# Optimization experiments

Measured on AMD Instinct MI355X. Metric: run time of the kernel, lower is better.

The kernel has to match this reference:

```python
import jax, jax.numpy as jnp
import numpy as np

SEQ, B, H, NP, HN = 2048, 2, 2048, 16, 128
SCALE = 1.0 / 11.313708498984761  # 1/sqrt(128), hardcoded in the source baddbmm


def setup_inputs() -> dict:
    key = jax.random.key(0)
    k1, k2, k3 = jax.random.split(key, 3)
    return {
        "hidden_states": jax.random.normal(k1, (SEQ, B, H), dtype=jnp.float32),
        "w_qkv": jax.random.normal(k2, (3 * H, H), dtype=jnp.float32) * 0.02,
        "w_out": jax.random.normal(k3, (H, H), dtype=jnp.float32) * 0.02,
    }


def reference(hidden_states, w_qkv, w_out):
    s, b, h = hidden_states.shape
    # QKV projection (column-parallel linear, no bias): [s, b, 3h]
    qkv = hidden_states @ w_qkv.T
    # [s, b, np, 3*hn] then split (num_query_groups == num_heads)
    qkv = qkv.reshape(s, b, NP, 3 * HN)
    q, k, v = qkv[..., :HN], qkv[..., HN:2 * HN], qkv[..., 2 * HN:]
    # baddbmm QK^T with alpha = 1/sqrt(128): scores [b, np, sq, sk]
    scores = jnp.einsum("sbnh,tbnh->bnst", q, k) * SCALE
    # scale_t == 1 then plain softmax (fallback path; no mask applied)
    prob = jax.nn.softmax(scores, axis=-1)
    # context: bmm(prob, V) -> [sq, b, np, hn] -> [sq, b, h]
    ctx = jnp.einsum("bnst,tbnh->sbnh", prob, v).reshape(s, b, h)
    # row-parallel output linear (no bias)
    return ctx @ w_out.T
```

## Files before the change

### kernel.cpp

```cpp
#include <hip/hip_runtime.h>
#include <stdint.h>

#define SEQ 2048
#define BATCH 2
#define HID 2048
#define NHEADS 16
#define HDIM 128
#define QKV_LD 6144
#define SCALE_F 0.08838834764831845f
#define LOG2E_F 1.4426950408889634f

typedef unsigned short u16;
using bf16x8 = __attribute__((ext_vector_type(8))) short;
using f32x4  = __attribute__((ext_vector_type(4))) float;

__device__ inline u16 f2bf(float f) {
  union { float f; uint32_t u; } c; c.f = f;
  uint32_t u = c.u;
  uint32_t r = (u + 0x7fffu + ((u >> 16) & 1u)) >> 16;
  return (u16)r;
}

__device__ inline void gl_lds16(const u16* g, u16* l) {
  __builtin_amdgcn_global_load_lds((const __attribute__((address_space(1))) void*)g,
                                   (__attribute__((address_space(3))) void*)l,
                                   16, 0, 0);
}

__global__ void cvt_all(const float* __restrict__ hs, const float* __restrict__ wqkv,
                        const float* __restrict__ wout, u16* __restrict__ ws_out) {
  int i = blockIdx.x * blockDim.x + threadIdx.x;
  const float* src;
  int j;
  float sc = 1.0f;
  if (i < 2097152) { src = hs; j = i; }
  else if (i < 5242880) {
    j = i - 2097152; src = wqkv;
    const int f = j >> 9;
    if ((f % 384) < 128) sc = SCALE_F;
  } else { j = i - 5242880; src = wout; }
  float4 v = ((const float4*)src)[j];
  ushort4 o;
  o.x = f2bf(v.x * sc); o.y = f2bf(v.y * sc); o.z = f2bf(v.z * sc); o.w = f2bf(v.w * sc);
  ((ushort4*)ws_out)[i] = o;
}

template<int MODE>
__global__ __launch_bounds__(256)
void gemm_bt(const u16* __restrict__ A, const u16* __restrict__ Bw,
             void* __restrict__ Cout, u16* __restrict__ vt, int M, int N, int K) {
  __shared__ __align__(16) u16 As[128 * 64];
  __shared__ __align__(16) u16 Bs[128 * 64];
  const int bm = blockIdx.x, bn = blockIdx.y;
  const int tid = threadIdx.x;
  const int wave = tid >> 6, lane = tid & 63;
  const int quad = lane >> 4, l16 = lane & 15;
  const int wm = (wave >> 1) * 64, wn = (wave & 1) * 64;
  f32x4 acc[4][4] = {};

  const u16* Ablk = A + (size_t)(bm * 128) * K;
  const u16* Bblk = Bw + (size_t)(bn * 128) * K;

  for (int k0 = 0; k0 < K; k0 += 64) {
    __syncthreads();
    #pragma unroll
    for (int p = 0; p < 4; ++p) {
      int j = p * 256 + tid;
      int r = j >> 3, cs = j & 7, c = cs ^ (r & 7);
      gl_lds16(Ablk + (size_t)r * K + k0 + c * 8, As + (p * 256 + wave * 64) * 8);
      gl_lds16(Bblk + (size_t)r * K + k0 + c * 8, Bs + (p * 256 + wave * 64) * 8);
    }
    __syncthreads();
    #pragma unroll
    for (int ks = 0; ks < 2; ++ks) {
      bf16x8 af[4], bfr[4];
      #pragma unroll
      for (int mt = 0; mt < 4; ++mt) {
        int row = wm + mt * 16 + l16;
        int cc = (ks * 4 + quad) ^ (row & 7);
        af[mt] = *(const bf16x8*)&As[(row * 8 + cc) * 8];
      }
      #pragma unroll
      for (int nt = 0; nt < 4; ++nt) {
        int row = wn + nt * 16 + l16;
        int cc = (ks * 4 + quad) ^ (row & 7);
        bfr[nt] = *(const bf16x8*)&Bs[(row * 8 + cc) * 8];
      }
      #pragma unroll
      for (int mt = 0; mt < 4; ++mt)
        #pragma unroll
        for (int nt = 0; nt < 4; ++nt)
          acc[mt][nt] = __builtin_amdgcn_mfma_f32_16x16x32_bf16(af[mt], bfr[nt], acc[mt][nt], 0, 0, 0);
    }
  }

  if (MODE == 1 && (bn % 3) == 2) {
    const int h = bn / 3;
    u16* vt0 = vt + ((size_t)h * HDIM) * SEQ;
    u16* vt1 = vt + ((size_t)(NHEADS + h) * HDIM) * SEQ;
    #pragma unroll
    for (int mt = 0; mt < 4; ++mt)
      #pragma unroll
      for (int nt = 0; nt < 4; ++nt) {
        const int hd = wn + nt * 16 + l16;
        const int s0 = (bm * 128 + wm + mt * 16 + quad * 4) >> 1;
        uint32_t w0 = (uint32_t)f2bf(acc[mt][nt][0]) | ((uint32_t)f2bf(acc[mt][nt][2]) << 16);
        uint32_t w1 = (uint32_t)f2bf(acc[mt][nt][1]) | ((uint32_t)f2bf(acc[mt][nt][3]) << 16);
        *(uint32_t*)&vt0[(size_t)hd * SEQ + s0] = w0;
        *(uint32_t*)&vt1[(size_t)hd * SEQ + s0] = w1;
      }
    return;
  }

  #pragma unroll
  for (int mt = 0; mt < 4; ++mt)
    #pragma unroll
    for (int nt = 0; nt < 4; ++nt)
      #pragma unroll
      for (int r = 0; r < 4; ++r) {
        int row = bm * 128 + wm + mt * 16 + quad * 4 + r;
        int col = bn * 128 + wn + nt * 16 + l16;
        float v = acc[mt][nt][r];
        if (MODE == 1) ((u16*)Cout)[(size_t)row * N + col] = f2bf(v);
        else           ((float*)Cout)[(size_t)row * N + col] = v;
      }
}

__global__ __launch_bounds__(512, 4)
void attn(const u16* __restrict__ qkv, const u16* __restrict__ vt_g, u16* __restrict__ ctx) {
  const int qt = blockIdx.x, head = blockIdx.y, b = blockIdx.z;
  const int q0 = qt * 128;
  __shared__ __align__(16) u16 Ks[64 * 128];
  __shared__ __align__(16) u16 Vt[144 * 64];
  __shared__ __align__(16) u16 PsT[128 * 64];
  const int tid = threadIdx.x;
  const int wave = tid >> 6, lane = tid & 63;
  const int quad = lane >> 4, l16 = lane & 15;

  const u16* qkv_bh = qkv + (size_t)b * QKV_LD + head * 384;
  const u16* vt = vt_g + (size_t)(b * NHEADS + head) * HDIM * SEQ;

  if (tid < 128) {
    const int row = 128 + (tid >> 3), c = tid & 7;
    const u16 v = (row == 128) ? (u16)0x3F80 : (u16)0;
    ushort4 q4; q4.x = v; q4.y = v; q4.z = v; q4.w = v;
    *(ushort4*)&Vt[(row * 8 + c) * 8] = q4;
    *(ushort4*)&Vt[(row * 8 + c) * 8 + 4] = q4;
  }

  bf16x8 qf[4];
  #pragma unroll
  for (int h = 0; h < 2; ++h) {
    __syncthreads();
    #pragma unroll
    for (int p = 0; p < 2; ++p) {
      int j = p * 512 + tid;
      int r = j >> 4, cs = j & 15, c = cs ^ (r & 7);
      gl_lds16(qkv_bh + (size_t)(q0 + h * 64 + r) * (BATCH * QKV_LD) + c * 8,
               Ks + (p * 512 + wave * 64) * 8);
    }
    __syncthreads();
    if ((wave >> 2) == h) {
      #pragma unroll
      for (int ks = 0; ks < 4; ++ks) {
        int row = (wave & 3) * 16 + l16;
        int cc = (ks * 4 + quad) ^ (row & 7);
        qf[ks] = *(const bf16x8*)&Ks[(row * 16 + cc) * 8];
      }
    }
  }

  f32x4 ot[9] = {};

  for (int kt = 0; kt < SEQ; kt += 64) {
    __syncthreads();
    #pragma unroll
    for (int p = 0; p < 2; ++p) {
      int j = p * 512 + tid;
      int r = j >> 4, cs = j & 15, c = cs ^ (r & 7);
      gl_lds16(qkv_bh + (size_t)(kt + r) * (BATCH * QKV_LD) + 128 + c * 8,
               Ks + (p * 512 + wave * 64) * 8);
    }
    #pragma unroll
    for (int p = 0; p < 2; ++p) {
      int j = p * 512 + tid;
      int hd = j >> 3, cs = j & 7, c = cs ^ (hd & 7);
      gl_lds16(vt + (size_t)hd * SEQ + kt + c * 8,
               Vt + (p * 512 + wave * 64) * 8);
    }
    __syncthreads();

    f32x4 st[4] = {};
    #pragma unroll
    for (int ks = 0; ks < 4; ++ks) {
      bf16x8 kf[4];
      #pragma unroll
      for (int mt = 0; mt < 4; ++mt) {
        int key = mt * 16 + l16;
        int cc = (ks * 4 + quad) ^ (key & 7);
        kf[mt] = *(const bf16x8*)&Ks[(key * 16 + cc) * 8];
      }
      #pragma unroll
      for (int mt = 0; mt < 4; ++mt)
        st[mt] = __builtin_amdgcn_mfma_f32_16x16x32_bf16(kf[mt], qf[ks], st[mt], 0, 0, 0);
    }

    #pragma unroll
    for (int mt = 0; mt < 4; ++mt) {
      ushort4 pk;
      union { float f; uint32_t u; } cv;
      cv.f = __builtin_amdgcn_exp2f(st[mt][0] * LOG2E_F); pk.x = (u16)(cv.u >> 16);
      cv.f = __builtin_amdgcn_exp2f(st[mt][1] * LOG2E_F); pk.y = (u16)(cv.u >> 16);
      cv.f = __builtin_amdgcn_exp2f(st[mt][2] * LOG2E_F); pk.z = (u16)(cv.u >> 16);
      cv.f = __builtin_amdgcn_exp2f(st[mt][3] * LOG2E_F); pk.w = (u16)(cv.u >> 16);
      const int q = wave * 16 + l16;
      const int kc = mt * 2 + (quad >> 1);
      *(ushort4*)&PsT[q * 64 + ((kc ^ (l16 & 7)) * 8 + (quad & 1) * 4)] = pk;
    }

    #pragma unroll
    for (int ks = 0; ks < 2; ++ks) {
      bf16x8 pf, vf[9];
      {
        const int q = wave * 16 + l16;
        const int cc = (ks * 4 + quad) ^ (l16 & 7);
        pf = *(const bf16x8*)&PsT[q * 64 + cc * 8];
      }
      #pragma unroll
      for (int mt = 0; mt < 9; ++mt) {
        const int hd = mt * 16 + l16;
        const int cc = (ks * 4 + quad) ^ (hd & 7);
        vf[mt] = *(const bf16x8*)&Vt[(hd * 8 + cc) * 8];
      }
      #pragma unroll
      for (int mt = 0; mt < 9; ++mt)
        ot[mt] = __builtin_amdgcn_mfma_f32_16x16x32_bf16(vf[mt], pf, ot[mt], 0, 0, 0);
    }
  }

  {
    const float lv = __shfl(ot[8][0], l16);
    const float inv_l = 1.0f / lv;
    const int s = q0 + wave * 16 + l16;
    u16* dst = ctx + ((size_t)s * BATCH + b) * HID + head * HDIM;
    #pragma unroll
    for (int mt = 0; mt < 8; ++mt) {
      ushort4 w;
      w.x = f2bf(ot[mt][0] * inv_l);
      w.y = f2bf(ot[mt][1] * inv_l);
      w.z = f2bf(ot[mt][2] * inv_l);
      w.w = f2bf(ot[mt][3] * inv_l);
      *(ushort4*)&dst[mt * 16 + quad * 4] = w;
    }
  }
}

extern "C" void kernel_launch(void* const* d_in, const int* in_sizes, int n_in,
                              void* d_out, int out_size, void* d_ws, size_t ws_size,
                              hipStream_t stream) {
  const float* hs   = (const float*)d_in[0];
  const float* wqkv = (const float*)d_in[1];
  const float* wout = (const float*)d_in[2];
  float* out = (float*)d_out;
  char* ws = (char*)d_ws;

  u16* hs_bf   = (u16*)(ws);
  u16* wqkv_bf = (u16*)(ws + 16777216);
  u16* wout_bf = (u16*)(ws + 41943040);
  u16* qkv_bf  = (u16*)(ws + 50331648);
  u16* vt_bf   = (u16*)(ws + 100663296);
  u16* ctx_bf  = hs_bf;

  cvt_all<<<24576, 256, 0, stream>>>(hs, wqkv, wout, (u16*)ws);

  gemm_bt<1><<<dim3(32, 48), 256, 0, stream>>>(hs_bf, wqkv_bf, qkv_bf, vt_bf, 4096, 6144, 2048);

  attn<<<dim3(16, NHEADS, BATCH), 512, 0, stream>>>(qkv_bf, vt_bf, ctx_bf);

  gemm_bt<0><<<dim3(32, 16), 256, 0, stream>>>(ctx_bf, wout_bf, out, nullptr, 4096, 2048, 2048);
}
```

Baseline: 393.5 us.

## Double-buffer K/V in attention with 256-query blocks and register row sums

```diff
diff --git a/kernel.cpp b/kernel.cpp
--- a/kernel.cpp
+++ b/kernel.cpp
@@ -126,13 +126,13 @@
       }
 }
 
-__global__ __launch_bounds__(512, 4)
+__global__ __launch_bounds__(1024, 4)
 void attn(const u16* __restrict__ qkv, const u16* __restrict__ vt_g, u16* __restrict__ ctx) {
   const int qt = blockIdx.x, head = blockIdx.y, b = blockIdx.z;
-  const int q0 = qt * 128;
-  __shared__ __align__(16) u16 Ks[64 * 128];
-  __shared__ __align__(16) u16 Vt[144 * 64];
-  __shared__ __align__(16) u16 PsT[128 * 64];
+  const int q0 = qt * 256;
+  __shared__ __align__(16) u16 Ks[2][64 * 128];
+  __shared__ __align__(16) u16 Vt[2][128 * 64];
+  __shared__ __align__(16) u16 PsT[256 * 64];
   const int tid = threadIdx.x;
   const int wave = tid >> 6, lane = tid & 63;
   const int quad = lane >> 4, l16 = lane & 15;
@@ -140,24 +140,15 @@
   const u16* qkv_bh = qkv + (size_t)b * QKV_LD + head * 384;
   const u16* vt = vt_g + (size_t)(b * NHEADS + head) * HDIM * SEQ;
 
-  if (tid < 128) {
-    const int row = 128 + (tid >> 3), c = tid & 7;
-    const u16 v = (row == 128) ? (u16)0x3F80 : (u16)0;
-    ushort4 q4; q4.x = v; q4.y = v; q4.z = v; q4.w = v;
-    *(ushort4*)&Vt[(row * 8 + c) * 8] = q4;
-    *(ushort4*)&Vt[(row * 8 + c) * 8 + 4] = q4;
-  }
-
   bf16x8 qf[4];
   #pragma unroll
-  for (int h = 0; h < 2; ++h) {
-    __syncthreads();
-    #pragma unroll
-    for (int p = 0; p < 2; ++p) {
-      int j = p * 512 + tid;
+  for (int h = 0; h < 4; ++h) {
+    __syncthreads();
+    {
+      int j = tid;
       int r = j >> 4, cs = j & 15, c = cs ^ (r & 7);
       gl_lds16(qkv_bh + (size_t)(q0 + h * 64 + r) * (BATCH * QKV_LD) + c * 8,
-               Ks + (p * 512 + wave * 64) * 8);
+               Ks[0] + (wave * 64) * 8);
     }
     __syncthreads();
     if ((wave >> 2) == h) {
@@ -165,30 +156,38 @@
       for (int ks = 0; ks < 4; ++ks) {
         int row = (wave & 3) * 16 + l16;
         int cc = (ks * 4 + quad) ^ (row & 7);
-        qf[ks] = *(const bf16x8*)&Ks[(row * 16 + cc) * 8];
-      }
-    }
-  }
-
-  f32x4 ot[9] = {};
-
-  for (int kt = 0; kt < SEQ; kt += 64) {
-    __syncthreads();
-    #pragma unroll
-    for (int p = 0; p < 2; ++p) {
-      int j = p * 512 + tid;
+        qf[ks] = *(const bf16x8*)&Ks[0][(row * 16 + cc) * 8];
+      }
+    }
+  }
+
+  auto stageKV = [&](int kt, int bb) {
+    {
+      int j = tid;
       int r = j >> 4, cs = j & 15, c = cs ^ (r & 7);
       gl_lds16(qkv_bh + (size_t)(kt + r) * (BATCH * QKV_LD) + 128 + c * 8,
-               Ks + (p * 512 + wave * 64) * 8);
-    }
-    #pragma unroll
-    for (int p = 0; p < 2; ++p) {
-      int j = p * 512 + tid;
+               Ks[bb] + (wave * 64) * 8);
+    }
+    {
+      int j = tid;
       int hd = j >> 3, cs = j & 7, c = cs ^ (hd & 7);
       gl_lds16(vt + (size_t)hd * SEQ + kt + c * 8,
-               Vt + (p * 512 + wave * 64) * 8);
-    }
-    __syncthreads();
+               Vt[bb] + (wave * 64) * 8);
+    }
+  };
+
+  f32x4 ot[8] = {};
+  float lacc = 0.0f;
+
+  __syncthreads();
+  stageKV(0, 0);
+  __syncthreads();
+
+  for (int it = 0; it < SEQ / 64; ++it) {
+    const int cur = it & 1;
+    if (it + 1 < SEQ / 64) stageKV((it + 1) * 64, cur ^ 1);
+    const u16* Kb = Ks[cur];
+    const u16* Vb = Vt[cur];
 
     f32x4 st[4] = {};
     #pragma unroll
@@ -198,21 +197,27 @@
       for (int mt = 0; mt < 4; ++mt) {
         int key = mt * 16 + l16;
         int cc = (ks * 4 + quad) ^ (key & 7);
-        kf[mt] = *(const bf16x8*)&Ks[(key * 16 + cc) * 8];
-      }
+        kf[mt] = *(const bf16x8*)&Kb[(key * 16 + cc) * 8];
+      }
+      __builtin_amdgcn_s_setprio(1);
       #pragma unroll
       for (int mt = 0; mt < 4; ++mt)
         st[mt] = __builtin_amdgcn_mfma_f32_16x16x32_bf16(kf[mt], qf[ks], st[mt], 0, 0, 0);
+      __builtin_amdgcn_s_setprio(0);
     }
 
     #pragma unroll
     for (int mt = 0; mt < 4; ++mt) {
       ushort4 pk;
-      union { float f; uint32_t u; } cv;
+      union { float f; uint32_t u; } cv, rv;
       cv.f = __builtin_amdgcn_exp2f(st[mt][0] * LOG2E_F); pk.x = (u16)(cv.u >> 16);
       cv.f = __builtin_amdgcn_exp2f(st[mt][1] * LOG2E_F); pk.y = (u16)(cv.u >> 16);
       cv.f = __builtin_amdgcn_exp2f(st[mt][2] * LOG2E_F); pk.z = (u16)(cv.u >> 16);
       cv.f = __builtin_amdgcn_exp2f(st[mt][3] * LOG2E_F); pk.w = (u16)(cv.u >> 16);
+      rv.u = (uint32_t)pk.x << 16; lacc += rv.f;
+      rv.u = (uint32_t)pk.y << 16; lacc += rv.f;
+      rv.u = (uint32_t)pk.z << 16; lacc += rv.f;
+      rv.u = (uint32_t)pk.w << 16; lacc += rv.f;
       const int q = wave * 16 + l16;
       const int kc = mt * 2 + (quad >> 1);
       *(ushort4*)&PsT[q * 64 + ((kc ^ (l16 & 7)) * 8 + (quad & 1) * 4)] = pk;
@@ -220,26 +225,32 @@
 
     #pragma unroll
     for (int ks = 0; ks < 2; ++ks) {
-      bf16x8 pf, vf[9];
+      bf16x8 pf, vf[8];
       {
         const int q = wave * 16 + l16;
         const int cc = (ks * 4 + quad) ^ (l16 & 7);
         pf = *(const bf16x8*)&PsT[q * 64 + cc * 8];
       }
       #pragma unroll
-      for (int mt = 0; mt < 9; ++mt) {
+      for (int mt = 0; mt < 8; ++mt) {
         const int hd = mt * 16 + l16;
         const int cc = (ks * 4 + quad) ^ (hd & 7);
-        vf[mt] = *(const bf16x8*)&Vt[(hd * 8 + cc) * 8];
-      }
-      #pragma unroll
-      for (int mt = 0; mt < 9; ++mt)
+        vf[mt] = *(const bf16x8*)&Vb[(hd * 8 + cc) * 8];
+      }
+      __builtin_amdgcn_s_setprio(1);
+      #pragma unroll
+      for (int mt = 0; mt < 8; ++mt)
         ot[mt] = __builtin_amdgcn_mfma_f32_16x16x32_bf16(vf[mt], pf, ot[mt], 0, 0, 0);
-    }
+      __builtin_amdgcn_s_setprio(0);
+    }
+
+    __syncthreads();
   }
 
   {
-    const float lv = __shfl(ot[8][0], l16);
+    float lv = lacc;
+    lv += __shfl_xor(lv, 16);
+    lv += __shfl_xor(lv, 32);
     const float inv_l = 1.0f / lv;
     const int s = q0 + wave * 16 + l16;
     u16* dst = ctx + ((size_t)s * BATCH + b) * HID + head * HDIM;
@@ -275,7 +286,7 @@
 
   gemm_bt<1><<<dim3(32, 48), 256, 0, stream>>>(hs_bf, wqkv_bf, qkv_bf, vt_bf, 4096, 6144, 2048);
 
-  attn<<<dim3(16, NHEADS, BATCH), 512, 0, stream>>>(qkv_bf, vt_bf, ctx_bf);
+  attn<<<dim3(8, NHEADS, BATCH), 1024, 0, stream>>>(qkv_bf, vt_bf, ctx_bf);
 
   gemm_bt<0><<<dim3(32, 16), 256, 0, stream>>>(ctx_bf, wout_bf, out, nullptr, 4096, 2048, 2048);
 }
```

New measurement: 372.9 us. 5.3% less time.
